# Kernel optimization log

Hardware: AMD Instinct MI355X
Metric: run time of the kernel (lower is better)

The kernel has to match this reference:

```python
import jax, jax.numpy as jnp
import numpy as np

# static config (matches init_kwargs and a standard 4-level FPN for ~800px input)
SPATIAL_SHAPES = ((100, 100), (50, 50), (25, 25), (13, 13))  # (H_l, W_l)
B, C, H, L, P = 2, 256, 8, 4, 4
DFFN = 2048
DH = C // H
LQ = sum(h * w for h, w in SPATIAL_SHAPES)  # 13294


def layer_norm(x, g, b, eps=1e-5):
    m = jnp.mean(x, -1, keepdims=True)
    v = jnp.mean((x - m) ** 2, -1, keepdims=True)
    return (x - m) * jax.lax.rsqrt(v + eps) * g + b


def ms_deform_sample(value, loc, attn):
    # value [B,Lv,H,DH], loc [B,Lq,H,L,P,2] in [0,1], attn [B,Lq,H,L,P]
    value = jnp.transpose(value, (0, 2, 1, 3))  # [B,H,Lv,DH]
    lq = loc.shape[1]
    out = jnp.zeros((B, H, lq, DH), value.dtype)
    start = 0
    for l, (Hl, Wl) in enumerate(SPATIAL_SHAPES):
        v = jax.lax.dynamic_slice_in_dim(value, start, Hl * Wl, axis=2)  # [B,H,N_l,DH]
        # grid_sample(align_corners=False) coords: x = loc_x*W - 0.5
        gx = jnp.transpose(loc[:, :, :, l, :, 0], (0, 2, 1, 3)) * Wl - 0.5  # [B,H,Lq,P]
        gy = jnp.transpose(loc[:, :, :, l, :, 1], (0, 2, 1, 3)) * Hl - 0.5
        aw = jnp.transpose(attn[:, :, :, l, :], (0, 2, 1, 3))  # [B,H,Lq,P]
        x0 = jnp.floor(gx)
        y0 = jnp.floor(gy)
        for dx in (0.0, 1.0):
            for dy in (0.0, 1.0):
                xi = x0 + dx
                yi = y0 + dy
                w = (1.0 - jnp.abs(gx - xi)) * (1.0 - jnp.abs(gy - yi))
                valid = (xi >= 0) & (xi < Wl) & (yi >= 0) & (yi < Hl)
                idx = (jnp.clip(yi, 0, Hl - 1) * Wl + jnp.clip(xi, 0, Wl - 1)).astype(jnp.int32)
                g = jnp.take_along_axis(v, idx.reshape(B, H, -1)[..., None], axis=2)  # [B,H,Lq*P,DH]
                ww = (w * aw * valid.astype(w.dtype))[..., None]  # [B,H,Lq,P,1]
                out = out + jnp.sum(g.reshape(B, H, lq, P, DH) * ww, axis=3)
        start += Hl * Wl
    return jnp.transpose(out, (0, 2, 1, 3)).reshape(B, lq, C)


def setup_inputs() -> dict:
    key = jax.random.key(0)
    ks = jax.random.split(key, 16)
    s = 0.02
    return {
        "src": jax.random.normal(ks[0], (B, LQ, C), jnp.float32),
        "pos": jax.random.normal(ks[1], (B, LQ, C), jnp.float32),
        "reference_points": jax.random.uniform(ks[2], (B, LQ, L, 2), jnp.float32),
        "w_value": jax.random.normal(ks[3], (C, C), jnp.float32) * s,
        "b_value": jnp.zeros((C,), jnp.float32),
        "w_off": jax.random.normal(ks[4], (C, H * L * P * 2), jnp.float32) * s,
        "b_off": jax.random.normal(ks[5], (H * L * P * 2,), jnp.float32) * s,
        "w_attn": jax.random.normal(ks[6], (C, H * L * P), jnp.float32) * s,
        "b_attn": jnp.zeros((H * L * P,), jnp.float32),
        "w_out": jax.random.normal(ks[7], (C, C), jnp.float32) * s,
        "b_out": jnp.zeros((C,), jnp.float32),
        "ln1_g": jnp.ones((C,), jnp.float32),
        "ln1_b": jnp.zeros((C,), jnp.float32),
        "w_ffn1": jax.random.normal(ks[8], (C, DFFN), jnp.float32) * s,
        "b_ffn1": jnp.zeros((DFFN,), jnp.float32),
        "w_ffn2": jax.random.normal(ks[9], (DFFN, C), jnp.float32) * s,
        "b_ffn2": jnp.zeros((C,), jnp.float32),
        "ln2_g": jnp.ones((C,), jnp.float32),
        "ln2_b": jnp.zeros((C,), jnp.float32),
    }


def reference(src, pos, reference_points, w_value, b_value, w_off, b_off, w_attn, b_attn,
              w_out, b_out, ln1_g, ln1_b, w_ffn1, b_ffn1, w_ffn2, b_ffn2, ln2_g, ln2_b):
    # DeformableTransformerEncoderLayer.forward (eval mode, no dropout)
    q = src + pos  # with_pos_embed
    lq = q.shape[1]
    value = (src @ w_value + b_value).reshape(B, -1, H, DH)
    off = (q @ w_off + b_off).reshape(B, lq, H, L, P, 2)
    attn = (q @ w_attn + b_attn).reshape(B, lq, H, L * P)
    attn = jax.nn.softmax(attn, axis=-1).reshape(B, lq, H, L, P)
    # offset_normalizer = (W_l, H_l)
    norm = jnp.array([[w, h] for h, w in SPATIAL_SHAPES], dtype=src.dtype)
    loc = reference_points[:, :, None, :, None, :] + off / norm[None, None, None, :, None, :]
    src2 = ms_deform_sample(value, loc, attn) @ w_out + b_out
    x = layer_norm(src + src2, ln1_g, ln1_b)
    ff = jax.nn.relu(x @ w_ffn1 + b_ffn1) @ w_ffn2 + b_ffn2
    return layer_norm(x + ff, ln2_g, ln2_b)
```

## Files before the change

### kernel.cpp

```cpp
#include <hip/hip_runtime.h>

#define LQN   13294
#define NBAT  2
#define MROWS (NBAT * LQN)
#define CCH   256
#define NHEAD 8
#define DHEAD 32
#define NLVL  4
#define NPT   4
#define DFF   2048

typedef short short8 __attribute__((ext_vector_type(8)));
typedef float f32x4 __attribute__((ext_vector_type(4)));
typedef unsigned short u16;
typedef u16 u16x4 __attribute__((ext_vector_type(4)));

__device__ __forceinline__ u16 f2bf(float f) {
  unsigned int u = __builtin_bit_cast(unsigned int, f);
  u += 0x7fffu + ((u >> 16) & 1u);
  return (u16)(u >> 16);
}
__device__ __forceinline__ float bf2f(u16 s) {
  unsigned int u = ((unsigned int)s) << 16;
  return __builtin_bit_cast(float, u);
}
__device__ __forceinline__ void async16(const void* g, void* l) {
  __builtin_amdgcn_global_load_lds(
      (const __attribute__((address_space(1))) void*)g,
      (__attribute__((address_space(3))) void*)l, 16, 0, 0);
}

template<int OUT_MODE>
__global__ __launch_bounds__(256, 2)
void gemm_bf16(const u16* __restrict__ A, const u16* __restrict__ BT,
               const float* __restrict__ bias, void* __restrict__ Cout,
               int M, int N, int K)
{
  __shared__ u16 As[2][128 * 64];
  __shared__ u16 Bs[2][128 * 64];
  const int t    = threadIdx.x;
  const int lane = t & 63;
  const int wid  = t >> 6;
  const int wm   = wid >> 1, wn = wid & 1;
  const int bm   = blockIdx.x, bn = blockIdx.y;
  const int l15  = lane & 15;
  const int kq   = lane >> 4;

  f32x4 acc[4][4];
#pragma unroll
  for (int m = 0; m < 4; ++m)
#pragma unroll
    for (int n = 0; n < 4; ++n) acc[m][n] = (f32x4)0.0f;

  auto stage = [&](int buf, int kt) {
#pragma unroll
    for (int i = 0; i < 4; ++i) {
      const int c   = i * 256 + t;
      const int row = c >> 3;
      const int kg  = (c & 7) ^ (row & 7);
      int ar = bm * 128 + row; ar = ar < M ? ar : M - 1;
      async16(&A[(size_t)ar * K + kt + kg * 8], &As[buf][c * 8]);
      const int br = bn * 128 + row;
      async16(&BT[(size_t)br * K + kt + kg * 8], &Bs[buf][c * 8]);
    }
  };

  stage(0, 0);
  __syncthreads();
  int cur = 0;

  for (int kt = 0; kt < K; kt += 64) {
    if (kt + 64 < K) stage(cur ^ 1, kt + 64);

#pragma unroll
    for (int kk = 0; kk < 2; ++kk) {
      short8 af[4], bfr[4];
#pragma unroll
      for (int m = 0; m < 4; ++m) {
        const int row = wm * 64 + m * 16 + l15;
        const int xb  = (kk * 64 + kq * 16) ^ ((row & 7) << 4);
        af[m] = *(const short8*)((const char*)&As[cur][0] + row * 128 + xb);
      }
#pragma unroll
      for (int n = 0; n < 4; ++n) {
        const int col = wn * 64 + n * 16 + l15;
        const int xb  = (kk * 64 + kq * 16) ^ ((col & 7) << 4);
        bfr[n] = *(const short8*)((const char*)&Bs[cur][0] + col * 128 + xb);
      }
#pragma unroll
      for (int m = 0; m < 4; ++m)
#pragma unroll
        for (int n = 0; n < 4; ++n)
          acc[m][n] = __builtin_amdgcn_mfma_f32_16x16x32_bf16(af[m], bfr[n], acc[m][n], 0, 0, 0);
    }

    __syncthreads();
    cur ^= 1;
  }

  const int crow0 = bm * 128 + wm * 64;
  const int ccol0 = bn * 128 + wn * 64;
#pragma unroll
  for (int n = 0; n < 4; ++n) {
    int col = ccol0 + n * 16 + l15;
    float bv = bias[col];
#pragma unroll
    for (int m = 0; m < 4; ++m) {
      int rbase = crow0 + m * 16 + kq * 4;
#pragma unroll
      for (int j = 0; j < 4; ++j) {
        int row = rbase + j;
        if (row < M) {
          float v = acc[m][n][j] + bv;
          if constexpr (OUT_MODE == 0) {
            ((float*)Cout)[(size_t)row * N + col] = v;
          } else {
            if constexpr (OUT_MODE == 2) v = fmaxf(v, 0.0f);
            ((u16*)Cout)[(size_t)row * N + col] = f2bf(v);
          }
        }
      }
    }
  }
}

__global__ __launch_bounds__(512, 2)
void ffn_fused(const u16* __restrict__ x_bf, const u16* __restrict__ W1T,
               const u16* __restrict__ W2T, const float* __restrict__ b1,
               const float* __restrict__ b2, float* __restrict__ out)
{
  extern __shared__ char smem[];
  u16* xs  = (u16*)(smem);
  u16* w1s = (u16*)(smem + 65536);
  u16* w2s = (u16*)(smem + 98304);
  u16* ps  = (u16*)(smem + 131072);

  const int t    = threadIdx.x;
  const int lane = t & 63;
  const int wid  = t >> 6;
  const int wm   = wid >> 2;
  const int wn   = wid & 3;
  const int l15  = lane & 15;
  const int kq   = lane >> 4;
  const int bm   = blockIdx.x;

#pragma unroll
  for (int i = 0; i < 8; ++i) {
    const int c   = i * 512 + t;
    const int row = c >> 5;
    const int kcs = (c & 31) ^ (row & 7);
    int ar = bm * 128 + row; ar = ar < MROWS ? ar : MROWS - 1;
    async16(&x_bf[(size_t)ar * 256 + kcs * 8], &xs[c * 8]);
  }

  f32x4 acc[4][4];
#pragma unroll
  for (int m = 0; m < 4; ++m)
#pragma unroll
    for (int n = 0; n < 4; ++n) acc[m][n] = (f32x4)0.0f;

  for (int it = 0; it < 32; ++it) {
#pragma unroll
    for (int i = 0; i < 4; ++i) {
      const int c  = i * 512 + t;
      const int r1 = c >> 5;
      const int k1 = ((c & 31) ^ (r1 & 7)) * 8;
      async16(&W1T[(size_t)(it * 64 + r1) * 256 + k1], &w1s[c * 8]);
      const int r2 = c >> 3;
      const int k2 = ((c & 7) ^ (r2 & 7)) * 8;
      async16(&W2T[(size_t)r2 * 2048 + it * 64 + k2], &w2s[c * 8]);
    }
    __syncthreads();

    f32x4 p[4];
#pragma unroll
    for (int m = 0; m < 4; ++m) p[m] = (f32x4)0.0f;
#pragma unroll
    for (int ks = 0; ks < 8; ++ks) {
      const int wrow = wn * 16 + l15;
      const int wxb  = (ks * 64 + kq * 16) ^ ((wrow & 7) << 4);
      const short8 bf = *(const short8*)((const char*)w1s + wrow * 512 + wxb);
#pragma unroll
      for (int m = 0; m < 4; ++m) {
        const int arow = wm * 64 + m * 16 + l15;
        const int axb  = (ks * 64 + kq * 16) ^ ((arow & 7) << 4);
        const short8 af = *(const short8*)((const char*)xs + arow * 512 + axb);
        p[m] = __builtin_amdgcn_mfma_f32_16x16x32_bf16(af, bf, p[m], 0, 0, 0);
      }
    }

    {
      const float bv = b1[it * 64 + wn * 16 + l15];
      const int pcol = wn * 16 + l15;
      const int chnk = pcol >> 3;
      const int sub  = (pcol & 7) * 2;
#pragma unroll
      for (int m = 0; m < 4; ++m)
#pragma unroll
        for (int j = 0; j < 4; ++j) {
          const int prow = wm * 64 + m * 16 + kq * 4 + j;
          const float v = fmaxf(p[m][j] + bv, 0.0f);
          *(u16*)((char*)ps + prow * 128 + ((chnk ^ (prow & 7)) * 16) + sub) = f2bf(v);
        }
    }
    __syncthreads();

#pragma unroll
    for (int kk = 0; kk < 2; ++kk) {
      short8 af[4], bfr[4];
#pragma unroll
      for (int m = 0; m < 4; ++m) {
        const int arow = wm * 64 + m * 16 + l15;
        const int axb  = ((kk * 4 + kq) ^ (arow & 7)) * 16;
        af[m] = *(const short8*)((const char*)ps + arow * 128 + axb);
      }
#pragma unroll
      for (int n = 0; n < 4; ++n) {
        const int brow = wn * 64 + n * 16 + l15;
        const int bxb  = ((kk * 4 + kq) ^ (brow & 7)) * 16;
        bfr[n] = *(const short8*)((const char*)w2s + brow * 128 + bxb);
      }
#pragma unroll
      for (int m = 0; m < 4; ++m)
#pragma unroll
        for (int n = 0; n < 4; ++n)
          acc[m][n] = __builtin_amdgcn_mfma_f32_16x16x32_bf16(af[m], bfr[n], acc[m][n], 0, 0, 0);
    }
    __syncthreads();
  }

  const int crow0 = bm * 128 + wm * 64;
#pragma unroll
  for (int n = 0; n < 4; ++n) {
    const int col = wn * 64 + n * 16 + l15;
    const float bv = b2[col];
#pragma unroll
    for (int m = 0; m < 4; ++m) {
      const int rbase = crow0 + m * 16 + kq * 4;
#pragma unroll
      for (int j = 0; j < 4; ++j) {
        const int row = rbase + j;
        if (row < MROWS) out[(size_t)row * 256 + col] = acc[m][n][j] + bv;
      }
    }
  }
}

__global__ __launch_bounds__(256)
void sampler_kernel(const float* __restrict__ offattn,
                    const float* __restrict__ refp,
                    const u16*  __restrict__ value,
                    u16*        __restrict__ src2)
{
  __shared__ float2 sWI[2][8][65];

  const int t   = threadIdx.x;
  const int r2  = t >> 7;
  const int g   = t & 127;
  const int row = blockIdx.x * 2 + r2;
  const int b   = row / LQN;

  {
    const int h   = g >> 4;
    const int p16 = g & 15;
    const int l   = p16 >> 2;

    const float* oa = offattn + (size_t)row * 384;

    float logit = oa[256 + h * 16 + p16];
    float mx = logit;
#pragma unroll
    for (int o = 1; o < 16; o <<= 1) mx = fmaxf(mx, __shfl_xor(mx, o, 64));
    float e = __expf(logit - mx);
    float s = e;
#pragma unroll
    for (int o = 1; o < 16; o <<= 1) s += __shfl_xor(s, o, 64);
    const float aw = e / s;

    const int Wl = (l == 0) ? 100 : (l == 1) ? 50 : (l == 2) ? 25 : 13;
    const int Hl = Wl;
    const int st = (l == 0) ? 0 : (l == 1) ? 10000 : (l == 2) ? 12500 : 13125;

    const float ox = oa[(h * 16 + p16) * 2 + 0];
    const float oy = oa[(h * 16 + p16) * 2 + 1];
    const float rx = refp[(size_t)row * 8 + l * 2 + 0] * (float)Wl - 0.5f;
    const float ry = refp[(size_t)row * 8 + l * 2 + 1] * (float)Hl - 0.5f;
    const float gx = rx + ox;
    const float gy = ry + oy;
    const float x0f = floorf(gx), y0f = floorf(gy);
    const int   x0 = (int)x0f, y0 = (int)y0f;
    const float fx = gx - x0f, fy = gy - y0f;

#pragma unroll
    for (int c = 0; c < 4; ++c) {
      const int dx = c & 1, dy = c >> 1;
      const int xi = x0 + dx, yi = y0 + dy;
      const float wx = dx ? fx : 1.0f - fx;
      const float wy = dy ? fy : 1.0f - fy;
      const bool valid = (xi >= 0) && (xi < Wl) && (yi >= 0) && (yi < Hl);
      const int xc = min(max(xi, 0), Wl - 1);
      const int yc = min(max(yi, 0), Hl - 1);
      const int idx = st + yc * Wl + xc;
      const float w = wx * wy * aw * (valid ? 1.0f : 0.0f);
      sWI[r2][h][p16 * 4 + c] = make_float2(w, __builtin_bit_cast(float, idx));
    }
  }
  __syncthreads();

  {
    const int h  = g >> 4;
    const int c2 = g & 15;
    const char* vbase = (const char*)value + (size_t)b * LQN * 512 + h * 64 + c2 * 4;
    const float2* wi = sWI[r2][h];

    float acc0 = 0.f, acc1 = 0.f;
#pragma unroll 16
    for (int e = 0; e < 64; ++e) {
      const float2 p = wi[e];
      const float w  = p.x;
      const int  idx = __builtin_bit_cast(int, p.y);
      const unsigned u = *(const unsigned*)(vbase + (size_t)idx * 512);
      const float f0 = __builtin_bit_cast(float, u << 16);
      const float f1 = __builtin_bit_cast(float, u & 0xffff0000u);
      acc0 += f0 * w;
      acc1 += f1 * w;
    }
    const unsigned o = (unsigned)f2bf(acc0) | ((unsigned)f2bf(acc1) << 16);
    *(unsigned*)&src2[(size_t)row * 256 + h * 32 + c2 * 2] = o;
  }
}

template<int WRITE_BF>
__global__ __launch_bounds__(256)
void ln_kernel(const float* __restrict__ Xa, const float* __restrict__ Xb,
               const float* __restrict__ gam, const float* __restrict__ bet,
               float* __restrict__ Yf, u16* __restrict__ Ybf)
{
  const int wid = threadIdx.x >> 6, lane = threadIdx.x & 63;
  const int row = blockIdx.x * 4 + wid;
  const f32x4 va = ((const f32x4*)(Xa + (size_t)row * 256))[lane];
  const f32x4 vb = ((const f32x4*)(Xb + (size_t)row * 256))[lane];
  f32x4 v = va + vb;
  float s1 = v[0] + v[1] + v[2] + v[3];
  float s2 = v[0] * v[0] + v[1] * v[1] + v[2] * v[2] + v[3] * v[3];
#pragma unroll
  for (int off = 32; off; off >>= 1) {
    s1 += __shfl_xor(s1, off, 64);
    s2 += __shfl_xor(s2, off, 64);
  }
  const float mean = s1 * (1.0f / 256.0f);
  const float var  = s2 * (1.0f / 256.0f) - mean * mean;
  const float rstd = rsqrtf(var + 1e-5f);
  const f32x4 gv = ((const f32x4*)gam)[lane];
  const f32x4 bv = ((const f32x4*)bet)[lane];
  f32x4 y;
#pragma unroll
  for (int j = 0; j < 4; ++j) y[j] = (v[j] - mean) * rstd * gv[j] + bv[j];
  ((f32x4*)(Yf + (size_t)row * 256))[lane] = y;
  if constexpr (WRITE_BF) {
    u16x4 o;
#pragma unroll
    for (int j = 0; j < 4; ++j) o[j] = f2bf(y[j]);
    ((u16x4*)(Ybf + (size_t)row * 256))[lane] = o;
  }
}

__global__ __launch_bounds__(256)
void prep_qsrc(const float* __restrict__ src, const float* __restrict__ pos,
               u16* __restrict__ src_bf, u16* __restrict__ q_bf)
{
  const size_t i = (size_t)blockIdx.x * 256 + threadIdx.x;
  const f32x4 s = ((const f32x4*)src)[i];
  const f32x4 p = ((const f32x4*)pos)[i];
  u16x4 sb, qb;
#pragma unroll
  for (int j = 0; j < 4; ++j) { sb[j] = f2bf(s[j]); qb[j] = f2bf(s[j] + p[j]); }
  ((u16x4*)src_bf)[i] = sb;
  ((u16x4*)q_bf)[i]   = qb;
}

__global__ __launch_bounds__(256)
void transpose_cast(const float* __restrict__ W, u16* __restrict__ WT, int K, int N)
{
  const int i = blockIdx.x * 256 + threadIdx.x;
  if (i >= K * N) return;
  const int k = i / N, n = i - k * N;
  WT[(size_t)n * K + k] = f2bf(W[i]);
}

__global__ __launch_bounds__(256)
void concat_bias(const float* __restrict__ b_off, const float* __restrict__ b_attn,
                 float* __restrict__ out)
{
  const int i = blockIdx.x * 256 + threadIdx.x;
  if (i < 256) out[i] = b_off[i];
  else if (i < 384) out[i] = b_attn[i - 256];
}

extern "C" void kernel_launch(void* const* d_in, const int* in_sizes, int n_in,
                              void* d_out, int out_size, void* d_ws, size_t ws_size,
                              hipStream_t stream)
{
  const float* src     = (const float*)d_in[0];
  const float* pos     = (const float*)d_in[1];
  const float* refp    = (const float*)d_in[2];
  const float* w_value = (const float*)d_in[3];
  const float* b_value = (const float*)d_in[4];
  const float* w_off   = (const float*)d_in[5];
  const float* b_off   = (const float*)d_in[6];
  const float* w_attn  = (const float*)d_in[7];
  const float* b_attn  = (const float*)d_in[8];
  const float* w_out   = (const float*)d_in[9];
  const float* b_out   = (const float*)d_in[10];
  const float* ln1_g   = (const float*)d_in[11];
  const float* ln1_b   = (const float*)d_in[12];
  const float* w_ffn1  = (const float*)d_in[13];
  const float* b_ffn1  = (const float*)d_in[14];
  const float* w_ffn2  = (const float*)d_in[15];
  const float* b_ffn2  = (const float*)d_in[16];
  const float* ln2_g   = (const float*)d_in[17];
  const float* ln2_b   = (const float*)d_in[18];

  char* ws = (char*)d_ws;
  size_t off = 0;
  auto alloc = [&](size_t bytes) { void* p = ws + off; off += (bytes + 255) & ~(size_t)255; return p; };

  u16*   src_bf   = (u16*)  alloc((size_t)MROWS * 256 * 2);
  u16*   q_bf     = (u16*)  alloc((size_t)MROWS * 256 * 2);
  float* offattn  = (float*)alloc((size_t)MROWS * 384 * 4);
  u16*   value_bf = (u16*)  alloc((size_t)MROWS * 256 * 2);
  u16*   src2_bf  = (u16*)  alloc((size_t)MROWS * 256 * 2);
  float* x_f32    = (float*)alloc((size_t)MROWS * 256 * 4);
  u16*   WT_val   = (u16*)  alloc(256 * 256 * 2);
  u16*   WT_oa    = (u16*)  alloc(384 * 256 * 2);
  u16*   WT_out   = (u16*)  alloc(256 * 256 * 2);
  u16*   WT_f1    = (u16*)  alloc(2048 * 256 * 2);
  u16*   WT_f2    = (u16*)  alloc((size_t)256 * 2048 * 2);
  float* bias_oa  = (float*)alloc(384 * 4);

  float* src2p = offattn;
  u16*   x_bf  = q_bf;
  float* ff    = (float*)value_bf;

  transpose_cast<<<256, 256, 0, stream>>>(w_value, WT_val, 256, 256);
  transpose_cast<<<256, 256, 0, stream>>>(w_off, WT_oa, 256, 256);
  transpose_cast<<<128, 256, 0, stream>>>(w_attn, WT_oa + 256 * 256, 256, 128);
  transpose_cast<<<256, 256, 0, stream>>>(w_out, WT_out, 256, 256);
  transpose_cast<<<2048, 256, 0, stream>>>(w_ffn1, WT_f1, 256, 2048);
  transpose_cast<<<2048, 256, 0, stream>>>(w_ffn2, WT_f2, 2048, 256);
  concat_bias<<<2, 256, 0, stream>>>(b_off, b_attn, bias_oa);

  prep_qsrc<<<6647, 256, 0, stream>>>(src, pos, src_bf, q_bf);

  gemm_bf16<1><<<dim3(208, 2), 256, 0, stream>>>(src_bf, WT_val, b_value, value_bf, MROWS, 256, 256);
  gemm_bf16<0><<<dim3(208, 3), 256, 0, stream>>>(q_bf, WT_oa, bias_oa, offattn, MROWS, 384, 256);

  sampler_kernel<<<MROWS / 2, 256, 0, stream>>>(offattn, refp, value_bf, src2_bf);

  gemm_bf16<0><<<dim3(208, 2), 256, 0, stream>>>(src2_bf, WT_out, b_out, src2p, MROWS, 256, 256);

  ln_kernel<1><<<6647, 256, 0, stream>>>(src, src2p, ln1_g, ln1_b, x_f32, x_bf);

  static bool attr_set = false;
  if (!attr_set) {
    hipFuncSetAttribute((const void*)ffn_fused,
                        hipFuncAttributeMaxDynamicSharedMemorySize, 147456);
    attr_set = true;
  }
  ffn_fused<<<208, 512, 147456, stream>>>(x_bf, WT_f1, WT_f2, b_ffn1, b_ffn2, ff);

  ln_kernel<0><<<6647, 256, 0, stream>>>(x_f32, ff, ln2_g, ln2_b, (float*)d_out, nullptr);
}
```

Measured before the change: 287.9 us.

## Double-buffer FFN weight tiles and keep X operand in registers

The fused FFN kernel now holds each block's X rows in registers instead of shared memory. That frees LDS for double-buffered W1/W2 tiles, so the next tile's loads are issued while the current tile computes. The first GEMM is remapped to a 4x2 warp grid with 2x2 MFMA tiles per warp, and the P buffer gets a padded 160-byte row stride with a new swizzle to cut bank conflicts. The costs are heavier register pressure from the X fragments, which may hurt occupancy at 512 threads, and a slightly larger shared memory allocation.

```diff
diff --git a/kernel.cpp b/kernel.cpp
--- a/kernel.cpp
+++ b/kernel.cpp
@@ -130,101 +130,115 @@
                const float* __restrict__ b2, float* __restrict__ out)
 {
   extern __shared__ char smem[];
-  u16* xs  = (u16*)(smem);
-  u16* w1s = (u16*)(smem + 65536);
-  u16* w2s = (u16*)(smem + 98304);
-  u16* ps  = (u16*)(smem + 131072);
+  u16* w1s = (u16*)(smem);
+  u16* w2s = (u16*)(smem + 65536);
+  char* ps = (char*)(smem + 131072);
 
   const int t    = threadIdx.x;
   const int lane = t & 63;
   const int wid  = t >> 6;
-  const int wm   = wid >> 2;
-  const int wn   = wid & 3;
   const int l15  = lane & 15;
   const int kq   = lane >> 4;
   const int bm   = blockIdx.x;
-
-#pragma unroll
-  for (int i = 0; i < 8; ++i) {
-    const int c   = i * 512 + t;
-    const int row = c >> 5;
-    const int kcs = (c & 31) ^ (row & 7);
-    int ar = bm * 128 + row; ar = ar < MROWS ? ar : MROWS - 1;
-    async16(&x_bf[(size_t)ar * 256 + kcs * 8], &xs[c * 8]);
-  }
-
-  f32x4 acc[4][4];
-#pragma unroll
-  for (int m = 0; m < 4; ++m)
-#pragma unroll
-    for (int n = 0; n < 4; ++n) acc[m][n] = (f32x4)0.0f;
-
-  for (int it = 0; it < 32; ++it) {
+  const int pwm  = wid >> 1, pwn = wid & 1;
+  const int wm   = wid >> 2, wn = wid & 3;
+
+  short8 xr[2][8];
+#pragma unroll
+  for (int m = 0; m < 2; ++m) {
+    int ar = bm * 128 + pwm * 32 + m * 16 + l15;
+    ar = ar < MROWS ? ar : MROWS - 1;
+    const char* xb = (const char*)x_bf + (size_t)ar * 512 + kq * 16;
+#pragma unroll
+    for (int ks = 0; ks < 8; ++ks)
+      xr[m][ks] = *(const short8*)(xb + ks * 64);
+  }
+
+  auto stage = [&](int buf, int it) {
 #pragma unroll
     for (int i = 0; i < 4; ++i) {
       const int c  = i * 512 + t;
       const int r1 = c >> 5;
       const int k1 = ((c & 31) ^ (r1 & 7)) * 8;
-      async16(&W1T[(size_t)(it * 64 + r1) * 256 + k1], &w1s[c * 8]);
+      async16(&W1T[(size_t)(it * 64 + r1) * 256 + k1], &w1s[buf * 16384 + c * 8]);
       const int r2 = c >> 3;
       const int k2 = ((c & 7) ^ (r2 & 7)) * 8;
-      async16(&W2T[(size_t)r2 * 2048 + it * 64 + k2], &w2s[c * 8]);
+      async16(&W2T[(size_t)r2 * 2048 + it * 64 + k2], &w2s[buf * 16384 + c * 8]);
+    }
+  };
+
+  f32x4 acc[4][4];
+#pragma unroll
+  for (int m = 0; m < 4; ++m)
+#pragma unroll
+    for (int n = 0; n < 4; ++n) acc[m][n] = (f32x4)0.0f;
+
+  stage(0, 0);
+  __syncthreads();
+
+  for (int it = 0; it < 32; ++it) {
+    const int cur = it & 1;
+    if (it < 31) stage(cur ^ 1, it + 1);
+
+    f32x4 p[2][2];
+#pragma unroll
+    for (int m = 0; m < 2; ++m)
+#pragma unroll
+      for (int n = 0; n < 2; ++n) p[m][n] = (f32x4)0.0f;
+
+#pragma unroll
+    for (int ks = 0; ks < 8; ++ks) {
+      short8 bfr[2];
+#pragma unroll
+      for (int n = 0; n < 2; ++n) {
+        const int wrow = pwn * 32 + n * 16 + l15;
+        const int xb   = (ks * 64 + kq * 16) ^ ((wrow & 7) << 4);
+        bfr[n] = *(const short8*)((const char*)&w1s[cur * 16384] + wrow * 512 + xb);
+      }
+#pragma unroll
+      for (int m = 0; m < 2; ++m)
+#pragma unroll
+        for (int n = 0; n < 2; ++n)
+          p[m][n] = __builtin_amdgcn_mfma_f32_16x16x32_bf16(xr[m][ks], bfr[n], p[m][n], 0, 0, 0);
+    }
+
+#pragma unroll
+    for (int n = 0; n < 2; ++n) {
+      const int col = pwn * 32 + n * 16 + l15;
+      const float bv = b1[it * 64 + col];
+      const int chnk = col >> 3;
+      const int sub  = (col & 7) * 2;
+#pragma unroll
+      for (int m = 0; m < 2; ++m)
+#pragma unroll
+        for (int j = 0; j < 4; ++j) {
+          const int prow = pwm * 32 + m * 16 + kq * 4 + j;
+          const float v = fmaxf(p[m][n][j] + bv, 0.0f);
+          *(u16*)(ps + prow * 160 + ((chnk ^ ((prow >> 2) & 3)) << 4) + sub) = f2bf(v);
+        }
     }
     __syncthreads();
 
-    f32x4 p[4];
-#pragma unroll
-    for (int m = 0; m < 4; ++m) p[m] = (f32x4)0.0f;
-#pragma unroll
-    for (int ks = 0; ks < 8; ++ks) {
-      const int wrow = wn * 16 + l15;
-      const int wxb  = (ks * 64 + kq * 16) ^ ((wrow & 7) << 4);
-      const short8 bf = *(const short8*)((const char*)w1s + wrow * 512 + wxb);
+#pragma unroll
+    for (int kk = 0; kk < 2; ++kk) {
+      short8 paf[4], bfr[4];
 #pragma unroll
       for (int m = 0; m < 4; ++m) {
         const int arow = wm * 64 + m * 16 + l15;
-        const int axb  = (ks * 64 + kq * 16) ^ ((arow & 7) << 4);
-        const short8 af = *(const short8*)((const char*)xs + arow * 512 + axb);
-        p[m] = __builtin_amdgcn_mfma_f32_16x16x32_bf16(af, bf, p[m], 0, 0, 0);
-      }
-    }
-
-    {
-      const float bv = b1[it * 64 + wn * 16 + l15];
-      const int pcol = wn * 16 + l15;
-      const int chnk = pcol >> 3;
-      const int sub  = (pcol & 7) * 2;
-#pragma unroll
-      for (int m = 0; m < 4; ++m)
-#pragma unroll
-        for (int j = 0; j < 4; ++j) {
-          const int prow = wm * 64 + m * 16 + kq * 4 + j;
-          const float v = fmaxf(p[m][j] + bv, 0.0f);
-          *(u16*)((char*)ps + prow * 128 + ((chnk ^ (prow & 7)) * 16) + sub) = f2bf(v);
-        }
-    }
-    __syncthreads();
-
-#pragma unroll
-    for (int kk = 0; kk < 2; ++kk) {
-      short8 af[4], bfr[4];
-#pragma unroll
-      for (int m = 0; m < 4; ++m) {
-        const int arow = wm * 64 + m * 16 + l15;
-        const int axb  = ((kk * 4 + kq) ^ (arow & 7)) * 16;
-        af[m] = *(const short8*)((const char*)ps + arow * 128 + axb);
+        const int c    = kk * 4 + kq;
+        paf[m] = *(const short8*)(ps + arow * 160 + ((c ^ ((arow >> 2) & 3)) << 4));
       }
 #pragma unroll
       for (int n = 0; n < 4; ++n) {
         const int brow = wn * 64 + n * 16 + l15;
-        const int bxb  = ((kk * 4 + kq) ^ (brow & 7)) * 16;
-        bfr[n] = *(const short8*)((const char*)w2s + brow * 128 + bxb);
+        const int xb   = ((kk * 4 + kq) ^ (brow & 7)) * 16;
+        bfr[n] = *(const short8*)((const char*)&w2s[cur * 16384] + brow * 128 + xb);
       }
 #pragma unroll
       for (int m = 0; m < 4; ++m)
 #pragma unroll
         for (int n = 0; n < 4; ++n)
-          acc[m][n] = __builtin_amdgcn_mfma_f32_16x16x32_bf16(af[m], bfr[n], acc[m][n], 0, 0, 0);
+          acc[m][n] = __builtin_amdgcn_mfma_f32_16x16x32_bf16(paf[m], bfr[n], acc[m][n], 0, 0, 0);
     }
     __syncthreads();
   }
@@ -464,10 +478,10 @@
   static bool attr_set = false;
   if (!attr_set) {
     hipFuncSetAttribute((const void*)ffn_fused,
-                        hipFuncAttributeMaxDynamicSharedMemorySize, 147456);
+                        hipFuncAttributeMaxDynamicSharedMemorySize, 151552);
     attr_set = true;
   }
-  ffn_fused<<<208, 512, 147456, stream>>>(x_bf, WT_f1, WT_f2, b_ffn1, b_ffn2, ff);
+  ffn_fused<<<208, 512, 151552, stream>>>(x_bf, WT_f1, WT_f2, b_ffn1, b_ffn2, ff);
 
   ln_kernel<0><<<6647, 256, 0, stream>>>(x_f32, ff, ln2_g, ln2_b, (float*)d_out, nullptr);
 }
```

After: 252.3 us. 1.14x faster.
